# Optimization experiments

Hardware: AMD Instinct MI355X
Metric: run time of the kernel (lower is better)

The kernel has to match this reference:

```python
import jax, jax.numpy as jnp
import numpy as np

B, S, D_EMB, D_HEAD = 4, 4096, 1024, 64

def setup_inputs() -> dict:
    key = jax.random.key(0)
    kx, kq, kk, kv = jax.random.split(key, 4)
    x = jax.random.normal(kx, (B, S, D_EMB), dtype=jnp.float32)
    # Linear(d_emb -> d_head, bias=False); stored as [d_emb, d_head] so y = x @ W
    sc = 1.0 / np.sqrt(D_EMB)
    Wq = jax.random.normal(kq, (D_EMB, D_HEAD), dtype=jnp.float32) * sc
    Wk = jax.random.normal(kk, (D_EMB, D_HEAD), dtype=jnp.float32) * sc
    Wv = jax.random.normal(kv, (D_EMB, D_HEAD), dtype=jnp.float32) * sc
    return {"x": x, "Wq": Wq, "Wk": Wk, "Wv": Wv}

def reference(x, Wq, Wk, Wv):
    # x: [B, S, D_EMB]
    n = x.shape[1]
    d_head = Wq.shape[1]
    q = x @ Wq  # [B, S, d_head]
    k = x @ Wk
    v = x @ Wv
    w = jnp.einsum('bqd,bkd->bqk', q, k)  # raw scores [B, S, S]
    causal = jnp.tril(jnp.ones((n, n), dtype=bool))
    w = jnp.where(causal[None, :, :], w, -jnp.inf)
    # NOTE: original scales AFTER masking (-inf * scale stays -inf, so math matches SDPA)
    scale = jnp.asarray(d_head, w.dtype) ** -0.5
    w = jax.nn.softmax(w * scale, axis=-1)
    # dropout_p = 0.0 (eval-mode reference)
    return w @ v  # [B, S, d_head]
```

## Files before the change

### kernel.cpp

```cpp
#include <hip/hip_runtime.h>

typedef __attribute__((ext_vector_type(4))) float f32x4;
typedef __attribute__((ext_vector_type(8))) short bf16x8;

#define S_LEN 4096

__device__ inline short f2bf(float f) {
    union { float f; unsigned u; } v; v.f = f;
    unsigned r = (v.u + 0x7fffu + ((v.u >> 16) & 1u)) >> 16;
    return (short)r;
}
__device__ inline unsigned pack2bf(float a, float b) {
    return (unsigned)(unsigned short)f2bf(a) | ((unsigned)(unsigned short)f2bf(b) << 16);
}
__device__ inline unsigned cvt_pk_bf16(float lo, float hi) {
    unsigned r;
    asm("v_cvt_pk_bf16_f32 %0, %1, %2" : "=v"(r) : "v"(lo), "v"(hi));
    return r;
}
__device__ inline void gload_lds16(const void* g, void* l) {
    __builtin_amdgcn_global_load_lds(
        (const __attribute__((address_space(1))) unsigned int*)g,
        (__attribute__((address_space(3))) unsigned int*)l, 16, 0, 0);
}

__global__ __launch_bounds__(256) void wconv_kernel(const float* __restrict__ Wq,
        const float* __restrict__ Wk, const float* __restrict__ Wv,
        short* __restrict__ Wsz) {
    int idx = blockIdx.x * 256 + threadIdx.x;
    int t = idx / 6144;
    int rem = idx - t * 6144;
    int c4 = rem / 1536;
    int rem2 = rem - c4 * 1536;
    int g = rem2 >> 3, e = rem2 & 7;
    int k = t * 32 + c4 * 8 + e;
    int m = g >> 6, c = g & 63;
    const float* W = (m == 0) ? Wq : (m == 1) ? Wk : Wv;
    Wsz[idx] = f2bf(W[k * 64 + c]);
}

__global__ __launch_bounds__(256, 2) void qkv_kernel(const float* __restrict__ x,
        const short* __restrict__ Wsz, short* __restrict__ Qb,
        short* __restrict__ Ksz, short* __restrict__ Vsz) {
    __shared__ __align__(16) char lds[3][16384];
    const int tid = threadIdx.x;
    const int wv = tid >> 6, lane = tid & 63;
    const int wr = wv & 1, wc = wv >> 1;
    const int lr = lane & 15, lg = lane >> 4;
    const int rowbase = blockIdx.x * 32;

    f32x4 acc[6];
#pragma unroll
    for (int i = 0; i < 6; i++) acc[i] = {0.f, 0.f, 0.f, 0.f};

    const int arow = tid >> 3, acL = tid & 7;
    const char* asrc = (const char*)(x + (size_t)(rowbase + arow) * 1024
                                     + ((acL ^ (arow & 7)) << 2));
    const char* wsrc = (const char*)Wsz + tid * 16;

#define STAGE(t_, s_)                                                       \
    {                                                                       \
        char* base_ = lds[(s_)];                                            \
        gload_lds16(asrc + (t_) * 128, base_ + tid * 16);                   \
        const char* bs_ = wsrc + (t_) * 12288;                              \
        gload_lds16(bs_,        base_ + 4096 + tid * 16);                   \
        gload_lds16(bs_ + 4096, base_ + 8192 + tid * 16);                   \
        gload_lds16(bs_ + 8192, base_ + 12288 + tid * 16);                  \
    }

    STAGE(0, 0);
    STAGE(1, 1);

    const int rowA = wr * 16 + lr;
    const int aswz = rowA & 7;

#pragma unroll
    for (int t = 0; t < 32; t++) {
        if (t < 31) asm volatile("s_waitcnt vmcnt(4)" ::: "memory");
        else        asm volatile("s_waitcnt vmcnt(0)" ::: "memory");
        __builtin_amdgcn_sched_barrier(0);
        __builtin_amdgcn_s_barrier();
        __builtin_amdgcn_sched_barrier(0);
        if (t + 2 < 32) STAGE(t + 2, (t + 2) % 3);

        const char* Ab = lds[t % 3];
        const char* Bb = lds[t % 3] + 4096;

        f32x4 a0 = *(const f32x4*)(Ab + rowA * 128 + (((lg * 2) ^ aswz) << 4));
        f32x4 a1 = *(const f32x4*)(Ab + rowA * 128 + (((lg * 2 + 1) ^ aswz) << 4));
        union { unsigned u[4]; bf16x8 v; } au;
        au.u[0] = cvt_pk_bf16(a0[0], a0[1]);
        au.u[1] = cvt_pk_bf16(a0[2], a0[3]);
        au.u[2] = cvt_pk_bf16(a1[0], a1[1]);
        au.u[3] = cvt_pk_bf16(a1[2], a1[3]);

#pragma unroll
        for (int cf = 0; cf < 6; cf++) {
            int brow = wc * 96 + cf * 16 + lr;
            bf16x8 b = *(const bf16x8*)(Bb + lg * 3072 + brow * 16);
            acc[cf] = __builtin_amdgcn_mfma_f32_16x16x32_bf16(au.v, b, acc[cf], 0, 0, 0);
        }
    }
#undef STAGE

#pragma unroll
    for (int cf = 0; cf < 6; cf++) {
        int gcol = wc * 96 + cf * 16 + lr;
        int m = gcol >> 6, cm = gcol & 63;
#pragma unroll
        for (int r = 0; r < 4; r++) {
            int row = rowbase + wr * 16 + lg * 4 + r;
            short bv = f2bf(acc[cf][r]);
            if (m == 0) {
                Qb[(size_t)row * 64 + cm] = bv;
            } else if (m == 1) {
                int b = row >> 12, s12 = row & 4095;
                int tk = s12 >> 6, rr = s12 & 63;
                Ksz[(((size_t)(b * 64 + tk) * 64 + rr) << 6)
                    + (((cm >> 3) ^ (rr & 7)) << 3) + (cm & 7)] = bv;
            } else {
                int b = row >> 12, s12 = row & 4095;
                int tk = s12 >> 6, kk = s12 & 63;
                Vsz[(((size_t)(b * 64 + tk) * 64 + cm) << 6)
                    + (((kk >> 3) ^ (cm & 7)) << 3) + (kk & 7)] = bv;
            }
        }
    }
}

__global__ __launch_bounds__(256, 3) void attn_fused_kernel(const short* __restrict__ Qb,
        const short* __restrict__ Ksz, const short* __restrict__ Vsz,
        float* __restrict__ o_part, float* __restrict__ m_part, float* __restrict__ l_part) {
    __shared__ __align__(16) char kvb2[2][16384];
    __shared__ __align__(16) char Pl[4 * 4096];
    const int tid = threadIdx.x;
    const int wv = tid >> 6, lane = tid & 63;
    const int lr = lane & 15, lg = lane >> 4;

    const int j = blockIdx.x;
    const int bb = j / 272;
    int jb = j - bb * 272;
    int qt = 0;
    while (jb >= ((qt + 2) >> 1)) { jb -= (qt + 2) >> 1; qt++; }
    const int c = jb;
    const int t0 = c * 4;
    const int nb = min(4, 2 * qt + 2 - 4 * c);
    const int qb_w = qt * 128 + wv * 32;

    bf16x8 qa[2][2];
#pragma unroll
    for (int qf = 0; qf < 2; qf++)
#pragma unroll
        for (int dk = 0; dk < 2; dk++)
            qa[qf][dk] = *(const bf16x8*)(Qb + (size_t)(bb * S_LEN + qb_w + qf * 16 + lr) * 64 + dk * 32 + lg * 8);

    f32x4 o[2][4];
    float mrun[2] = {-1e30f, -1e30f}, lrun[2] = {0.f, 0.f};
#pragma unroll
    for (int qf = 0; qf < 2; qf++)
#pragma unroll
        for (int df = 0; df < 4; df++) o[qf][df] = {0.f, 0.f, 0.f, 0.f};

    const char* Kg = (const char*)Ksz;
    const char* Vg = (const char*)Vsz;
    char* Pb = Pl + wv * 4096;

#define STAGEKV(t_, s_)                                                       \
    {                                                                         \
        size_t off_ = (size_t)(bb * 64 + t0 + (t_)) * 8192 + tid * 16;        \
        char* d_ = kvb2[(s_)] + tid * 16;                                     \
        gload_lds16(Kg + off_,        d_);                                    \
        gload_lds16(Kg + off_ + 4096, d_ + 4096);                             \
        gload_lds16(Vg + off_,        d_ + 8192);                             \
        gload_lds16(Vg + off_ + 4096, d_ + 12288);                            \
    }

    STAGEKV(0, 0);
    asm volatile("s_waitcnt vmcnt(0)" ::: "memory");
    __builtin_amdgcn_s_barrier();

    for (int t = 0; t < nb; t++) {
        if (t + 1 < nb) STAGEKV(t + 1, (t + 1) & 1);

        const int kv0 = (t0 + t) * 64;
        if (kv0 <= qb_w + 31) {
            const char* Kl = kvb2[t & 1];
            const char* Vl = Kl + 8192;

            bf16x8 kb[4][2], vb[2][4];
#pragma unroll
            for (int kf = 0; kf < 4; kf++)
#pragma unroll
                for (int dk = 0; dk < 2; dk++) {
                    int r = kf * 16 + lr;
                    kb[kf][dk] = *(const bf16x8*)(Kl + r * 128 + ((((dk << 2) | lg) ^ (r & 7)) << 4));
                }
#pragma unroll
            for (int kk = 0; kk < 2; kk++)
#pragma unroll
                for (int df = 0; df < 4; df++) {
                    int d = df * 16 + lr;
                    vb[kk][df] = *(const bf16x8*)(Vl + d * 128 + ((((kk << 2) | lg) ^ (d & 7)) << 4));
                }

            f32x4 s[2][4];
#pragma unroll
            for (int qf = 0; qf < 2; qf++)
#pragma unroll
                for (int kf = 0; kf < 4; kf++) {
                    f32x4 z = {0.f, 0.f, 0.f, 0.f};
                    z = __builtin_amdgcn_mfma_f32_16x16x32_bf16(kb[kf][0], qa[qf][0], z, 0, 0, 0);
                    s[qf][kf] = __builtin_amdgcn_mfma_f32_16x16x32_bf16(kb[kf][1], qa[qf][1], z, 0, 0, 0);
                }

            const bool needmask = (kv0 + 63) > qb_w;
#pragma unroll
            for (int qf = 0; qf < 2; qf++)
#pragma unroll
                for (int kf = 0; kf < 4; kf++)
#pragma unroll
                    for (int r = 0; r < 4; r++) {
                        float v = s[qf][kf][r] * 0.125f;
                        if (needmask) {
                            int row = qb_w + qf * 16 + lr;
                            int col = kv0 + kf * 16 + lg * 4 + r;
                            if (col > row) v = -1e30f;
                        }
                        s[qf][kf][r] = v;
                    }

#pragma unroll
            for (int qf = 0; qf < 2; qf++) {
                float pm = -1e30f;
#pragma unroll
                for (int kf = 0; kf < 4; kf++)
#pragma unroll
                    for (int r = 0; r < 4; r++) pm = fmaxf(pm, s[qf][kf][r]);
                pm = fmaxf(pm, __shfl_xor(pm, 16, 64));
                pm = fmaxf(pm, __shfl_xor(pm, 32, 64));
                float mnew = fmaxf(mrun[qf], pm);
                float fac = __expf(mrun[qf] - mnew);
                mrun[qf] = mnew;

                const int q = qf * 16 + lr;
                const int swz = (q & 7) << 4;
                float rs = 0.f;
#pragma unroll
                for (int kf = 0; kf < 4; kf++) {
                    float p0 = __expf(s[qf][kf][0] - mnew);
                    float p1 = __expf(s[qf][kf][1] - mnew);
                    float p2 = __expf(s[qf][kf][2] - mnew);
                    float p3 = __expf(s[qf][kf][3] - mnew);
                    rs += (p0 + p1) + (p2 + p3);
                    uint2 w; w.x = pack2bf(p0, p1); w.y = pack2bf(p2, p3);
                    int byt = (q * 128 + kf * 32 + lg * 8) ^ swz;
                    *(uint2*)(Pb + byt) = w;
                }
                rs += __shfl_xor(rs, 16, 64);
                rs += __shfl_xor(rs, 32, 64);
                lrun[qf] = lrun[qf] * fac + rs;
#pragma unroll
                for (int df = 0; df < 4; df++)
#pragma unroll
                    for (int r = 0; r < 4; r++) o[qf][df][r] *= fac;
            }

            bf16x8 pa[2][2];
#pragma unroll
            for (int qf = 0; qf < 2; qf++)
#pragma unroll
                for (int kk = 0; kk < 2; kk++) {
                    int q = qf * 16 + lr;
                    int byt = (q * 128 + kk * 64 + lg * 16) ^ ((q & 7) << 4);
                    pa[qf][kk] = *(const bf16x8*)(Pb + byt);
                }

#pragma unroll
            for (int qf = 0; qf < 2; qf++)
#pragma unroll
                for (int df = 0; df < 4; df++) {
                    o[qf][df] = __builtin_amdgcn_mfma_f32_16x16x32_bf16(vb[0][df], pa[qf][0], o[qf][df], 0, 0, 0);
                    o[qf][df] = __builtin_amdgcn_mfma_f32_16x16x32_bf16(vb[1][df], pa[qf][1], o[qf][df], 0, 0, 0);
                }
        }

        asm volatile("s_waitcnt vmcnt(0)" ::: "memory");
        __builtin_amdgcn_sched_barrier(0);
        __builtin_amdgcn_s_barrier();
    }
#undef STAGEKV

#pragma unroll
    for (int qf = 0; qf < 2; qf++)
#pragma unroll
        for (int df = 0; df < 4; df++)
            *(f32x4*)(o_part + ((size_t)j * 128 + wv * 32 + qf * 16 + lr) * 64 + df * 16 + lg * 4) = o[qf][df];
    if (lg == 0) {
#pragma unroll
        for (int qf = 0; qf < 2; qf++) {
            m_part[(size_t)j * 128 + wv * 32 + qf * 16 + lr] = mrun[qf];
            l_part[(size_t)j * 128 + wv * 32 + qf * 16 + lr] = lrun[qf];
        }
    }
}

__global__ __launch_bounds__(256) void combine_kernel(const float* __restrict__ o_part,
        const float* __restrict__ m_part, const float* __restrict__ l_part,
        float* __restrict__ out) {
    const int idx = blockIdx.x * 256 + threadIdx.x;
    const int col = idx & 63;
    const int rowg = idx >> 6;
    const int bb = rowg >> 12;
    const int srow = rowg & 4095;
    const int qt = srow >> 7;
    const int rloc = srow & 127;
    const int h = qt >> 1;
    const int n = (qt + 2) >> 1;
    const int jb0 = bb * 272 + h * (h + 1) + (qt & 1) * (h + 1);

    float M = -1e30f;
    for (int cc = 0; cc < n; cc++) M = fmaxf(M, m_part[(size_t)(jb0 + cc) * 128 + rloc]);
    float L = 0.f, acc = 0.f;
    for (int cc = 0; cc < n; cc++) {
        float w = __expf(m_part[(size_t)(jb0 + cc) * 128 + rloc] - M);
        L += l_part[(size_t)(jb0 + cc) * 128 + rloc] * w;
        acc += o_part[((size_t)(jb0 + cc) * 128 + rloc) * 64 + col] * w;
    }
    out[idx] = acc / L;
}

extern "C" void kernel_launch(void* const* d_in, const int* in_sizes, int n_in,
                              void* d_out, int out_size, void* d_ws, size_t ws_size,
                              hipStream_t stream) {
    const float* x  = (const float*)d_in[0];
    const float* Wq = (const float*)d_in[1];
    const float* Wk = (const float*)d_in[2];
    const float* Wv = (const float*)d_in[3];
    float* out = (float*)d_out;

    char* ws = (char*)d_ws;
    short* Wsz = (short*)(ws);
    short* Qb  = (short*)(ws + 0x60000);
    short* Ksz = (short*)(ws + 0x260000);
    short* Vsz = (short*)(ws + 0x460000);

    const int njobs = 1088;
    float* o_part = (float*)(ws + 0x660000);
    float* m_part = o_part + (size_t)njobs * 128 * 64;
    float* l_part = m_part + (size_t)njobs * 128;

    hipLaunchKernelGGL(wconv_kernel, dim3(768), dim3(256), 0, stream, Wq, Wk, Wv, Wsz);
    hipLaunchKernelGGL(qkv_kernel,  dim3(512), dim3(256), 0, stream, x, Wsz, Qb, Ksz, Vsz);
    hipLaunchKernelGGL(attn_fused_kernel, dim3(njobs), dim3(256), 0, stream,
                       Qb, Ksz, Vsz, o_part, m_part, l_part);
    hipLaunchKernelGGL(combine_kernel, dim3(4096), dim3(256), 0, stream,
                       o_part, m_part, l_part, out);
}
```

Before: 71.48 us.

## Preload bf16 x row panel into LDS and halve QKV rows per block

The QKV projection kernel now loads each block's entire 16-row fp32 x panel up front, converts it once to bf16, and stores it in a swizzled LDS panel. Only the bf16 weights are streamed through the triple-buffered pipeline. Rows per block drop from 32 to 16 and the grid doubles to 1024 blocks, with each wave owning 48 output columns. This removes per-step x streaming and conversion and adds parallelism, but the x load is synchronous, not overlapped, and each weight tile is now reused across fewer rows, so total weight traffic doubles.

```diff
diff --git a/kernel.cpp b/kernel.cpp
--- a/kernel.cpp
+++ b/kernel.cpp
@@ -42,74 +42,78 @@
 __global__ __launch_bounds__(256, 2) void qkv_kernel(const float* __restrict__ x,
         const short* __restrict__ Wsz, short* __restrict__ Qb,
         short* __restrict__ Ksz, short* __restrict__ Vsz) {
-    __shared__ __align__(16) char lds[3][16384];
+    __shared__ __align__(16) char Apan[32768];
+    __shared__ __align__(16) char Bl[3][12288];
     const int tid = threadIdx.x;
     const int wv = tid >> 6, lane = tid & 63;
-    const int wr = wv & 1, wc = wv >> 1;
     const int lr = lane & 15, lg = lane >> 4;
-    const int rowbase = blockIdx.x * 32;
-
-    f32x4 acc[6];
-#pragma unroll
-    for (int i = 0; i < 6; i++) acc[i] = {0.f, 0.f, 0.f, 0.f};
-
-    const int arow = tid >> 3, acL = tid & 7;
-    const char* asrc = (const char*)(x + (size_t)(rowbase + arow) * 1024
-                                     + ((acL ^ (arow & 7)) << 2));
+    const int rowbase = blockIdx.x * 16;
+
+    {
+        const int row = tid >> 4, i = tid & 15;
+        const float* src = x + (size_t)(rowbase + row) * 1024;
+        char* dstbase = Apan + row * 2048;
+#pragma unroll
+        for (int j = 0; j < 16; j++) {
+            int u = j * 16 + i;
+            f32x4 v = *(const f32x4*)(src + u * 4);
+            uint2 w;
+            w.x = cvt_pk_bf16(v[0], v[1]);
+            w.y = cvt_pk_bf16(v[2], v[3]);
+            int c = u >> 1, sub = u & 1;
+            *(uint2*)(dstbase + (((c ^ (row & 7)) << 4) | (sub << 3))) = w;
+        }
+    }
+    __syncthreads();
+
+    f32x4 acc[3];
+#pragma unroll
+    for (int i = 0; i < 3; i++) acc[i] = {0.f, 0.f, 0.f, 0.f};
+
     const char* wsrc = (const char*)Wsz + tid * 16;
 
 #define STAGE(t_, s_)                                                       \
     {                                                                       \
-        char* base_ = lds[(s_)];                                            \
-        gload_lds16(asrc + (t_) * 128, base_ + tid * 16);                   \
+        char* base_ = Bl[(s_)];                                             \
         const char* bs_ = wsrc + (t_) * 12288;                              \
-        gload_lds16(bs_,        base_ + 4096 + tid * 16);                   \
-        gload_lds16(bs_ + 4096, base_ + 8192 + tid * 16);                   \
-        gload_lds16(bs_ + 8192, base_ + 12288 + tid * 16);                  \
+        gload_lds16(bs_,        base_ + tid * 16);                          \
+        gload_lds16(bs_ + 4096, base_ + 4096 + tid * 16);                   \
+        gload_lds16(bs_ + 8192, base_ + 8192 + tid * 16);                   \
     }
 
     STAGE(0, 0);
     STAGE(1, 1);
 
-    const int rowA = wr * 16 + lr;
-    const int aswz = rowA & 7;
-
 #pragma unroll
     for (int t = 0; t < 32; t++) {
-        if (t < 31) asm volatile("s_waitcnt vmcnt(4)" ::: "memory");
+        if (t < 31) asm volatile("s_waitcnt vmcnt(3)" ::: "memory");
         else        asm volatile("s_waitcnt vmcnt(0)" ::: "memory");
         __builtin_amdgcn_sched_barrier(0);
         __builtin_amdgcn_s_barrier();
         __builtin_amdgcn_sched_barrier(0);
         if (t + 2 < 32) STAGE(t + 2, (t + 2) % 3);
 
-        const char* Ab = lds[t % 3];
-        const char* Bb = lds[t % 3] + 4096;
-
-        f32x4 a0 = *(const f32x4*)(Ab + rowA * 128 + (((lg * 2) ^ aswz) << 4));
-        f32x4 a1 = *(const f32x4*)(Ab + rowA * 128 + (((lg * 2 + 1) ^ aswz) << 4));
-        union { unsigned u[4]; bf16x8 v; } au;
-        au.u[0] = cvt_pk_bf16(a0[0], a0[1]);
-        au.u[1] = cvt_pk_bf16(a0[2], a0[3]);
-        au.u[2] = cvt_pk_bf16(a1[0], a1[1]);
-        au.u[3] = cvt_pk_bf16(a1[2], a1[3]);
-
-#pragma unroll
-        for (int cf = 0; cf < 6; cf++) {
-            int brow = wc * 96 + cf * 16 + lr;
+        const char* Bb = Bl[t % 3];
+
+        bf16x8 a = *(const bf16x8*)(Apan + lr * 2048
+                                    + (((t * 4 + lg) ^ (lr & 7)) << 4));
+
+#pragma unroll
+        for (int cf = 0; cf < 3; cf++) {
+            int brow = wv * 48 + cf * 16 + lr;
             bf16x8 b = *(const bf16x8*)(Bb + lg * 3072 + brow * 16);
-            acc[cf] = __builtin_amdgcn_mfma_f32_16x16x32_bf16(au.v, b, acc[cf], 0, 0, 0);
+            acc[cf] = __builtin_amdgcn_mfma_f32_16x16x32_bf16(a, b, acc[cf], 0, 0, 0);
         }
     }
 #undef STAGE
 
 #pragma unroll
-    for (int cf = 0; cf < 6; cf++) {
-        int gcol = wc * 96 + cf * 16 + lr;
+    for (int cf = 0; cf < 3; cf++) {
+        int gcol = wv * 48 + cf * 16 + lr;
         int m = gcol >> 6, cm = gcol & 63;
 #pragma unroll
         for (int r = 0; r < 4; r++) {
-            int row = rowbase + wr * 16 + lg * 4 + r;
+            int row = rowbase + lg * 4 + r;
             short bv = f2bf(acc[cf][r]);
             if (m == 0) {
                 Qb[(size_t)row * 64 + cm] = bv;
@@ -350,7 +354,7 @@
     float* l_part = m_part + (size_t)njobs * 128;
 
     hipLaunchKernelGGL(wconv_kernel, dim3(768), dim3(256), 0, stream, Wq, Wk, Wv, Wsz);
-    hipLaunchKernelGGL(qkv_kernel,  dim3(512), dim3(256), 0, stream, x, Wsz, Qb, Ksz, Vsz);
+    hipLaunchKernelGGL(qkv_kernel,  dim3(1024), dim3(256), 0, stream, x, Wsz, Qb, Ksz, Vsz);
     hipLaunchKernelGGL(attn_fused_kernel, dim3(njobs), dim3(256), 0, stream,
                        Qb, Ksz, Vsz, o_part, m_part, l_part);
     hipLaunchKernelGGL(combine_kernel, dim3(4096), dim3(256), 0, stream,
```

Result: slower. 98.68 us (+38.1%).
